# Optimization experiments

Measured on AMD Instinct MI355X. Metric: run time of the kernel, lower is better.

## Reference

```python
import jax, jax.numpy as jnp
import numpy as np

B, S, D = 4, 1024, 1024
H = 16
DH = D // H  # head dim = 64
SCALE = DH ** -0.5
NEG = -1e18


def setup_inputs() -> dict:
    key = jax.random.key(0)
    ks = jax.random.split(key, 8)
    queries = jax.random.normal(ks[0], (B, S, D), dtype=jnp.float32)
    keys_ = jax.random.normal(ks[1], (B, S, D), dtype=jnp.float32)
    values = jax.random.normal(ks[2], (B, S, D), dtype=jnp.float32)
    mask = jax.random.randint(ks[3], (B, 1, S), 0, 2).astype(bool)
    sd = 1.0 / np.sqrt(D)
    Wq = jax.random.normal(ks[4], (D, D), dtype=jnp.float32) * sd
    Wk = jax.random.normal(ks[5], (D, D), dtype=jnp.float32) * sd
    Wv = jax.random.normal(ks[6], (D, D), dtype=jnp.float32) * sd
    Wo = jax.random.normal(ks[7], (D, D), dtype=jnp.float32) * sd
    return {"queries": queries, "keys": keys_, "values": values,
            "Wq": Wq, "Wk": Wk, "Wv": Wv, "Wo": Wo, "mask": mask}


def _split_heads(x):
    # [B,S,D] -> [B,H,S,DH]
    b, s, d = x.shape
    return x.reshape(b, s, H, d // H).transpose(0, 2, 1, 3)


def reference(queries, keys, values, Wq, Wk, Wv, Wo, mask):
    q = _split_heads(queries @ Wq) * SCALE          # [B,H,S,DH]
    k = _split_heads(keys @ Wk)                     # [B,H,S,DH]
    v = _split_heads(values @ Wv)                   # [B,H,S,DH]
    logits = jnp.einsum('bhqd,bhkd->bhqk', q, k)    # [B,H,S,S]
    # mask [B,1,Lk] -> unsqueeze head dim -> broadcast over [B,H,Lq,Lk]
    logits = jnp.where(mask[:, None, :, :], NEG, logits)
    attention_weights = logits.sum(axis=1) / H      # [B,S,S] head-averaged logits
    w = jax.nn.softmax(logits, axis=-1)             # dropout p=0 -> identity
    ctx = jnp.einsum('bhqk,bhkd->bhqd', w, v)       # [B,H,S,DH]
    ctx = ctx.transpose(0, 2, 1, 3).reshape(q.shape[0], q.shape[2], H * DH)
    outputs = ctx @ Wo                              # [B,S,D]
    return (outputs, attention_weights)
```

## Files before the change

kernel.cpp:

```cpp
#include <hip/hip_runtime.h>
#include <hip/hip_bf16.h>

typedef __bf16 bf16;
typedef __attribute__((ext_vector_type(8))) __bf16 bf16x8;
typedef __attribute__((ext_vector_type(4))) __bf16 bf16x4;
typedef __attribute__((ext_vector_type(4))) float f32x4;

#define NEGV (-1e18f)
#define LOG2E 1.4426950408889634f

__device__ __forceinline__ bf16 f2b(float f) {
    unsigned u = __builtin_bit_cast(unsigned, f);
    u += 0x7fffu + ((u >> 16) & 1u);
    unsigned short h = (unsigned short)(u >> 16);
    return __builtin_bit_cast(bf16, h);
}

__device__ __forceinline__ f32x4 mfma16(bf16x8 a, bf16x8 b, f32x4 c) {
    return __builtin_amdgcn_mfma_f32_16x16x32_bf16(a, b, c, 0, 0, 0);
}

__device__ __forceinline__ void gl16(const void* g, void* l) {
    __builtin_amdgcn_global_load_lds((const __attribute__((address_space(1))) void*)g,
                                     (__attribute__((address_space(3))) void*)l, 16, 0, 0);
}

__global__ __launch_bounds__(256) void wconv(const float* __restrict__ W0,
                                             const float* __restrict__ W1,
                                             const float* __restrict__ W2,
                                             const float* __restrict__ W3,
                                             bf16* __restrict__ out) {
    __shared__ float tile[64][65];
    const float* Ws[4] = {W0, W1, W2, W3};
    const float* W = Ws[blockIdx.z];
    bf16* O = out + ((size_t)blockIdx.z << 20);
    int t = threadIdx.x;
    int k0 = blockIdx.x * 64, n0 = blockIdx.y * 64;
#pragma unroll
    for (int p = 0; p < 4; p++) {
        int r = (t >> 4) + p * 16, c = (t & 15) * 4;
        float4 v = *(const float4*)&W[(size_t)(k0 + r) * 1024 + n0 + c];
        tile[r][c] = v.x; tile[r][c + 1] = v.y; tile[r][c + 2] = v.z; tile[r][c + 3] = v.w;
    }
    __syncthreads();
#pragma unroll
    for (int p = 0; p < 4; p++) {
        int r = (t >> 4) + p * 16, c = (t & 15) * 4;
        bf16x4 o;
        o[0] = f2b(tile[c][r]); o[1] = f2b(tile[c + 1][r]);
        o[2] = f2b(tile[c + 2][r]); o[3] = f2b(tile[c + 3][r]);
        *(bf16x4*)&O[(size_t)(n0 + r) * 1024 + k0 + c] = o;
    }
}

__global__ __launch_bounds__(256, 3) void gemm_proj(const float* __restrict__ Qf,
                                                    const float* __restrict__ Kf,
                                                    const float* __restrict__ Vf,
                                                    const bf16* __restrict__ WtQ,
                                                    bf16* __restrict__ Qw,
                                                    bf16* __restrict__ Kw,
                                                    bf16* __restrict__ VtG) {
    __shared__ bf16 As[128 * 64];
    __shared__ bf16 Bs[128 * 64];
    char* AsB = (char*)As;
    char* BsB = (char*)Bs;
    int t = threadIdx.x;
    int m0 = blockIdx.x * 128, n0 = blockIdx.y * 128;
    int z = blockIdx.z;
    const float* A = (z == 0) ? Qf : (z == 1) ? Kf : Vf;
    const bf16* Bt = WtQ + ((size_t)z << 20);
    int wid = t >> 6, lane = t & 63;
    int wr = wid >> 1, wc = wid & 1, lr = lane & 15, lg = lane >> 4;
    f32x4 zero = {0.f, 0.f, 0.f, 0.f};
    f32x4 acc[4][4];
#pragma unroll
    for (int m = 0; m < 4; m++)
#pragma unroll
        for (int n = 0; n < 4; n++) acc[m][n] = zero;

    float4 pa[4][2];
#pragma unroll
    for (int i = 0; i < 4; i++) {
        int c = wid * 256 + i * 64 + lane;
        int row = c >> 3, q = c & 7;
        const float* src = &A[(size_t)(m0 + row) * 1024 + q * 8];
        pa[i][0] = *(const float4*)src;
        pa[i][1] = *(const float4*)(src + 4);
    }

    for (int k0 = 0; k0 < 1024; k0 += 64) {
        __syncthreads();
#pragma unroll
        for (int i = 0; i < 4; i++) {
            int c = wid * 256 + i * 64 + lane;
            int row = c >> 3, q = (c & 7) ^ (row & 7);
            gl16(&Bt[(size_t)(n0 + row) * 1024 + k0 + q * 8], (void*)&Bs[c * 8]);
        }
#pragma unroll
        for (int i = 0; i < 4; i++) {
            int c = wid * 256 + i * 64 + lane;
            int row = c >> 3;
            bf16x8 o;
            o[0] = f2b(pa[i][0].x); o[1] = f2b(pa[i][0].y);
            o[2] = f2b(pa[i][0].z); o[3] = f2b(pa[i][0].w);
            o[4] = f2b(pa[i][1].x); o[5] = f2b(pa[i][1].y);
            o[6] = f2b(pa[i][1].z); o[7] = f2b(pa[i][1].w);
            *(bf16x8*)(AsB + ((c * 16) ^ ((row & 7) << 4))) = o;
        }
        __syncthreads();
        if (k0 < 960) {
#pragma unroll
            for (int i = 0; i < 4; i++) {
                int c = wid * 256 + i * 64 + lane;
                int row = c >> 3, q = c & 7;
                const float* src = &A[(size_t)(m0 + row) * 1024 + k0 + 64 + q * 8];
                pa[i][0] = *(const float4*)src;
                pa[i][1] = *(const float4*)(src + 4);
            }
        }
#pragma unroll
        for (int kk = 0; kk < 2; kk++) {
            bf16x8 af[4], bfr[4];
#pragma unroll
            for (int m = 0; m < 4; m++) {
                int row = wr * 64 + m * 16 + lr;
                af[m] = *(const bf16x8*)(AsB + ((row * 128 + kk * 64 + lg * 16) ^ ((row & 7) << 4)));
            }
#pragma unroll
            for (int n = 0; n < 4; n++) {
                int row = wc * 64 + n * 16 + lr;
                bfr[n] = *(const bf16x8*)(BsB + ((row * 128 + kk * 64 + lg * 16) ^ ((row & 7) << 4)));
            }
#pragma unroll
            for (int m = 0; m < 4; m++)
#pragma unroll
                for (int n = 0; n < 4; n++) acc[m][n] = mfma16(af[m], bfr[n], acc[m][n]);
        }
    }
#pragma unroll
    for (int n = 0; n < 4; n++) {
        int colg = n0 + wc * 64 + n * 16 + lr;
#pragma unroll
        for (int m = 0; m < 4; m++) {
            int rowg = m0 + wr * 64 + m * 16 + lg * 4;
            if (z == 2) {
                bf16x4 o;
#pragma unroll
                for (int j = 0; j < 4; j++) o[j] = f2b(acc[m][n][j]);
                *(bf16x4*)&VtG[(size_t)colg * 4096 + rowg] = o;
            } else {
                bf16* C = (z == 0) ? Qw : Kw;
                float sc = (z == 0) ? 0.125f : 1.0f;
#pragma unroll
                for (int j = 0; j < 4; j++)
                    C[(size_t)(rowg + j) * 1024 + colg] = f2b(acc[m][n][j] * sc);
            }
        }
    }
}

__global__ __launch_bounds__(256, 3) void gemm_oa(const bf16* __restrict__ CTX,
                                                  const bf16* __restrict__ WtO,
                                                  float* __restrict__ out,
                                                  const bf16* __restrict__ Qw,
                                                  const bf16* __restrict__ Kw,
                                                  float* __restrict__ aw,
                                                  const int* __restrict__ maskp) {
    __shared__ bf16 As[128 * 64];
    __shared__ bf16 Bs[128 * 64];
    char* AsB = (char*)As;
    char* BsB = (char*)Bs;
    int t = threadIdx.x;
    int z = blockIdx.z;
    int bx = blockIdx.x;
    int m0, n0 = blockIdx.y * 128;
    const bf16* A;
    const bf16* Bt;
    float* C;
    const int* mask = nullptr;
    if (z == 0) {
        m0 = bx * 128;
        A = CTX; Bt = WtO; C = out;
    } else {
        int b = bx >> 3;
        m0 = (bx & 7) * 128;
        A = Qw + ((size_t)b << 20); Bt = Kw + ((size_t)b << 20);
        C = aw + ((size_t)b << 20); mask = maskp + b * 1024;
    }
    int wid = t >> 6, lane = t & 63;
    int wr = wid >> 1, wc = wid & 1, lr = lane & 15, lg = lane >> 4;
    f32x4 zero = {0.f, 0.f, 0.f, 0.f};
    f32x4 acc[4][4];
#pragma unroll
    for (int m = 0; m < 4; m++)
#pragma unroll
        for (int n = 0; n < 4; n++) acc[m][n] = zero;

    for (int k0 = 0; k0 < 1024; k0 += 64) {
        __syncthreads();
#pragma unroll
        for (int i = 0; i < 4; i++) {
            int c = wid * 256 + i * 64 + lane;
            int row = c >> 3, q = (c & 7) ^ (row & 7);
            gl16(&A[(size_t)(m0 + row) * 1024 + k0 + q * 8], (void*)&As[c * 8]);
            gl16(&Bt[(size_t)(n0 + row) * 1024 + k0 + q * 8], (void*)&Bs[c * 8]);
        }
        __syncthreads();
#pragma unroll
        for (int kk = 0; kk < 2; kk++) {
            bf16x8 af[4], bfr[4];
#pragma unroll
            for (int m = 0; m < 4; m++) {
                int row = wr * 64 + m * 16 + lr;
                af[m] = *(const bf16x8*)(AsB + ((row * 128 + kk * 64 + lg * 16) ^ ((row & 7) << 4)));
            }
#pragma unroll
            for (int n = 0; n < 4; n++) {
                int row = wc * 64 + n * 16 + lr;
                bfr[n] = *(const bf16x8*)(BsB + ((row * 128 + kk * 64 + lg * 16) ^ ((row & 7) << 4)));
            }
#pragma unroll
            for (int m = 0; m < 4; m++)
#pragma unroll
                for (int n = 0; n < 4; n++) acc[m][n] = mfma16(af[m], bfr[n], acc[m][n]);
        }
    }
#pragma unroll
    for (int n = 0; n < 4; n++) {
        int colg = n0 + wc * 64 + n * 16 + lr;
        int mk = (z == 1) ? mask[colg] : 0;
#pragma unroll
        for (int m = 0; m < 4; m++) {
            int rowg = m0 + wr * 64 + m * 16 + lg * 4;
#pragma unroll
            for (int j = 0; j < 4; j++) {
                float v = acc[m][n][j];
                size_t idx = (size_t)(rowg + j) * 1024 + colg;
                if (z == 0) C[idx] = v;
                else C[idx] = mk ? NEGV : v * (1.f / 16.f);
            }
        }
    }
}

__global__ __launch_bounds__(256, 4) void flash_k(const bf16* __restrict__ Q,
                                                  const bf16* __restrict__ K,
                                                  const bf16* __restrict__ VT,
                                                  bf16* __restrict__ CTX,
                                                  const int* __restrict__ maskp) {
    __shared__ bf16 Ks[64 * 64];
    __shared__ bf16 Vs[64 * 64];
    __shared__ bf16 Ps[4][16 * 64];
    __shared__ float biasS[1024];
    int bid = blockIdx.x;
    int qt = bid & 15, h = (bid >> 4) & 15, b = bid >> 8;
    int t = threadIdx.x, wid = t >> 6, lane = t & 63;
    int lr = lane & 15, lg = lane >> 4;
    int qbase = qt * 64 + wid * 16;
    const size_t bS = (size_t)b * 1024;
    char* KsB = (char*)Ks;
    char* VsB = (char*)Vs;
    char* PsW = (char*)&Ps[wid][0];
    const int sxl = (lr & 7) << 4;

    {
        int4 mv = *(const int4*)&maskp[b * 1024 + t * 4];
        float4 bv;
        const float NB = NEGV * LOG2E;
        bv.x = mv.x ? NB : 0.f; bv.y = mv.y ? NB : 0.f;
        bv.z = mv.z ? NB : 0.f; bv.w = mv.w ? NB : 0.f;
        *(float4*)&biasS[t * 4] = bv;
    }

    bf16x8 qf[2];
#pragma unroll
    for (int c = 0; c < 2; c++)
        qf[c] = *(const bf16x8*)&Q[(bS + qbase + lr) * 1024 + h * 64 + c * 32 + lg * 8];

    f32x4 zero = {0.f, 0.f, 0.f, 0.f};
    f32x4 acc[4];
#pragma unroll
    for (int d = 0; d < 4; d++) acc[d] = zero;
    float mr = -INFINITY;
    float lsum = 0.f;

    const bf16* Kbase = K + bS * 1024 + h * 64;
    const bf16* Vbase = VT + (size_t)(h * 64) * 4096 + bS;

    int c0 = t, c1 = t + 256;
    int kr0 = c0 >> 3, kq0 = c0 & 7, kr1 = c1 >> 3, kq1 = c1 & 7;

    bf16x8 kg[2], vg[2];
    kg[0] = *(const bf16x8*)&Kbase[(size_t)kr0 * 1024 + kq0 * 8];
    kg[1] = *(const bf16x8*)&Kbase[(size_t)kr1 * 1024 + kq1 * 8];
    vg[0] = *(const bf16x8*)&Vbase[(size_t)kr0 * 4096 + kq0 * 8];
    vg[1] = *(const bf16x8*)&Vbase[(size_t)kr1 * 4096 + kq1 * 8];

    for (int kt = 0; kt < 16; kt++) {
        __syncthreads();
        *(bf16x8*)(KsB + ((kr0 * 128 + kq0 * 16) ^ ((kr0 & 7) << 4))) = kg[0];
        *(bf16x8*)(KsB + ((kr1 * 128 + kq1 * 16) ^ ((kr1 & 7) << 4))) = kg[1];
        *(bf16x8*)(VsB + ((kr0 * 128 + kq0 * 16) ^ ((kr0 & 7) << 4))) = vg[0];
        *(bf16x8*)(VsB + ((kr1 * 128 + kq1 * 16) ^ ((kr1 & 7) << 4))) = vg[1];
        __syncthreads();
        if (kt < 15) {
            size_t ko = (size_t)(kt + 1) * 64;
            kg[0] = *(const bf16x8*)&Kbase[(ko + kr0) * 1024 + kq0 * 8];
            kg[1] = *(const bf16x8*)&Kbase[(ko + kr1) * 1024 + kq1 * 8];
            vg[0] = *(const bf16x8*)&Vbase[(size_t)kr0 * 4096 + ko + kq0 * 8];
            vg[1] = *(const bf16x8*)&Vbase[(size_t)kr1 * 4096 + ko + kq1 * 8];
        }
        f32x4 s[4];
        __builtin_amdgcn_s_setprio(1);
#pragma unroll
        for (int n = 0; n < 4; n++) {
            int row = n * 16 + lr;
            bf16x8 kf0 = *(const bf16x8*)(KsB + ((row * 128 + lg * 16) ^ sxl));
            bf16x8 kf1 = *(const bf16x8*)(KsB + ((row * 128 + 64 + lg * 16) ^ sxl));
            f32x4 zz = zero;
            zz = mfma16(kf0, qf[0], zz);
            zz = mfma16(kf1, qf[1], zz);
            s[n] = zz;
        }
        __builtin_amdgcn_s_setprio(0);
#pragma unroll
        for (int n = 0; n < 4; n++) {
            float4 bv = *(const float4*)&biasS[kt * 64 + n * 16 + lg * 4];
            s[n][0] = __builtin_fmaf(s[n][0], LOG2E, bv.x);
            s[n][1] = __builtin_fmaf(s[n][1], LOG2E, bv.y);
            s[n][2] = __builtin_fmaf(s[n][2], LOG2E, bv.z);
            s[n][3] = __builtin_fmaf(s[n][3], LOG2E, bv.w);
        }
        float pm;
        {
            float a0 = fmaxf(fmaxf(s[0][0], s[0][1]), fmaxf(s[0][2], s[0][3]));
            float a1 = fmaxf(fmaxf(s[1][0], s[1][1]), fmaxf(s[1][2], s[1][3]));
            float a2 = fmaxf(fmaxf(s[2][0], s[2][1]), fmaxf(s[2][2], s[2][3]));
            float a3 = fmaxf(fmaxf(s[3][0], s[3][1]), fmaxf(s[3][2], s[3][3]));
            pm = fmaxf(fmaxf(a0, a1), fmaxf(a2, a3));
        }
        pm = fmaxf(pm, __shfl_xor(pm, 16));
        pm = fmaxf(pm, __shfl_xor(pm, 32));
        float mn = fmaxf(mr, pm);
        float sc = __builtin_exp2f(mr - mn);
        mr = mn;
        float rs;
        {
            float r0 = 0.f, r1 = 0.f, r2 = 0.f, r3 = 0.f;
#pragma unroll
            for (int n = 0; n < 4; n++) {
                float p0 = __builtin_exp2f(s[n][0] - mn);
                float p1 = __builtin_exp2f(s[n][1] - mn);
                float p2 = __builtin_exp2f(s[n][2] - mn);
                float p3 = __builtin_exp2f(s[n][3] - mn);
                s[n][0] = p0; s[n][1] = p1; s[n][2] = p2; s[n][3] = p3;
                r0 += p0; r1 += p1; r2 += p2; r3 += p3;
            }
            rs = (r0 + r1) + (r2 + r3);
        }
        rs += __shfl_xor(rs, 16);
        rs += __shfl_xor(rs, 32);
        lsum = lsum * sc + rs;
        float scb[4];
#pragma unroll
        for (int j = 0; j < 4; j++) scb[j] = __shfl(sc, lg * 4 + j);
#pragma unroll
        for (int d = 0; d < 4; d++) {
            acc[d][0] *= scb[0]; acc[d][1] *= scb[1];
            acc[d][2] *= scb[2]; acc[d][3] *= scb[3];
        }
#pragma unroll
        for (int n = 0; n < 4; n++) {
            bf16x4 o;
            o[0] = (bf16)s[n][0]; o[1] = (bf16)s[n][1];
            o[2] = (bf16)s[n][2]; o[3] = (bf16)s[n][3];
            *(bf16x4*)(PsW + ((lr * 128 + n * 32 + lg * 8) ^ sxl)) = o;
        }
        __builtin_amdgcn_s_setprio(1);
#pragma unroll
        for (int c = 0; c < 2; c++) {
            bf16x8 pa = *(const bf16x8*)(PsW + ((lr * 128 + c * 64 + lg * 16) ^ sxl));
#pragma unroll
            for (int d = 0; d < 4; d++) {
                int row = d * 16 + lr;
                bf16x8 vb = *(const bf16x8*)(VsB + ((row * 128 + c * 64 + lg * 16) ^ ((row & 7) << 4)));
                acc[d] = mfma16(pa, vb, acc[d]);
            }
        }
        __builtin_amdgcn_s_setprio(0);
    }
    float lb[4];
#pragma unroll
    for (int j = 0; j < 4; j++) lb[j] = __shfl(lsum, lg * 4 + j);
#pragma unroll
    for (int j = 0; j < 4; j++) {
        float inv = 1.f / lb[j];
#pragma unroll
        for (int d = 0; d < 4; d++)
            CTX[(bS + qbase + lg * 4 + j) * 1024 + h * 64 + d * 16 + lr] = f2b(acc[d][j] * inv);
    }
}

extern "C" void kernel_launch(void* const* d_in, const int* in_sizes, int n_in,
                              void* d_out, int out_size, void* d_ws, size_t ws_size,
                              hipStream_t stream) {
    const float* queries = (const float*)d_in[0];
    const float* keys    = (const float*)d_in[1];
    const float* values  = (const float*)d_in[2];
    const float* Wq = (const float*)d_in[3];
    const float* Wk = (const float*)d_in[4];
    const float* Wv = (const float*)d_in[5];
    const float* Wo = (const float*)d_in[6];
    const int* mask = (const int*)d_in[7];

    float* out = (float*)d_out;
    float* aw  = out + ((size_t)4 << 20);

    bf16* wsb = (bf16*)d_ws;
    bf16* WtQ = wsb;
    bf16* Qw  = wsb + ((size_t)4 << 20);
    bf16* Kw  = wsb + ((size_t)8 << 20);
    bf16* VtG = wsb + ((size_t)12 << 20);
    bf16* CTX = wsb + ((size_t)16 << 20);

    wconv<<<dim3(16, 16, 4), 256, 0, stream>>>(Wq, Wk, Wv, Wo, WtQ);
    gemm_proj<<<dim3(32, 8, 3), 256, 0, stream>>>(queries, keys, values, WtQ, Qw, Kw, VtG);
    flash_k<<<dim3(1024), 256, 0, stream>>>(Qw, Kw, VtG, CTX, mask);
    gemm_oa<<<dim3(32, 8, 2), 256, 0, stream>>>(CTX, WtQ + ((size_t)3 << 20), out,
                                                Qw, Kw, aw, mask);
}
```

Baseline: 116.8 us.

## Double-buffer LDS tiles in projection and output GEMMs to overlap loads with MFMA

Both GEMM kernels now keep two LDS buffers for the A and B tiles. The next k-tile is staged into the alternate buffer while MFMAs run on the current one, which leaves one barrier per iteration instead of two. The extra shared memory lowers the launch-bounds occupancy hint from 3 to 2 blocks per CU. Overlap should hide global-to-LDS latency, at the cost of fewer resident waves.

```diff
diff --git a/kernel.cpp b/kernel.cpp
--- a/kernel.cpp
+++ b/kernel.cpp
@@ -53,17 +53,18 @@
     }
 }
 
-__global__ __launch_bounds__(256, 3) void gemm_proj(const float* __restrict__ Qf,
+__global__ __launch_bounds__(256, 2) void gemm_proj(const float* __restrict__ Qf,
                                                     const float* __restrict__ Kf,
                                                     const float* __restrict__ Vf,
                                                     const bf16* __restrict__ WtQ,
                                                     bf16* __restrict__ Qw,
                                                     bf16* __restrict__ Kw,
                                                     bf16* __restrict__ VtG) {
-    __shared__ bf16 As[128 * 64];
-    __shared__ bf16 Bs[128 * 64];
+    __shared__ bf16 As[2][128 * 64];
+    __shared__ bf16 Bs[2][128 * 64];
     char* AsB = (char*)As;
     char* BsB = (char*)Bs;
+    const int BUFSZ = 128 * 64 * 2;
     int t = threadIdx.x;
     int m0 = blockIdx.x * 128, n0 = blockIdx.y * 128;
     int z = blockIdx.z;
@@ -78,45 +79,55 @@
 #pragma unroll
         for (int n = 0; n < 4; n++) acc[m][n] = zero;
 
-    float4 pa[4][2];
+    int sc_[4], srow[4], sq[4];
 #pragma unroll
     for (int i = 0; i < 4; i++) {
         int c = wid * 256 + i * 64 + lane;
-        int row = c >> 3, q = c & 7;
-        const float* src = &A[(size_t)(m0 + row) * 1024 + q * 8];
-        pa[i][0] = *(const float4*)src;
-        pa[i][1] = *(const float4*)(src + 4);
-    }
-
+        sc_[i] = c; srow[i] = c >> 3; sq[i] = c & 7;
+    }
+
+    float4 pa[4][2];
+#define LOADA(K0)                                                              \
+    {                                                                          \
+        _Pragma("unroll") for (int i = 0; i < 4; i++) {                        \
+            const float* src = &A[(size_t)(m0 + srow[i]) * 1024 + (K0) + sq[i] * 8]; \
+            pa[i][0] = *(const float4*)src;                                    \
+            pa[i][1] = *(const float4*)(src + 4);                              \
+        }                                                                      \
+    }
+#define STAGE_B(BUF, K0)                                                       \
+    {                                                                          \
+        _Pragma("unroll") for (int i = 0; i < 4; i++) {                        \
+            int q = sq[i] ^ (srow[i] & 7);                                     \
+            gl16(&Bt[(size_t)(n0 + srow[i]) * 1024 + (K0) + q * 8],            \
+                 (void*)&Bs[BUF][sc_[i] * 8]);                                 \
+        }                                                                      \
+    }
+#define WRITE_A(BUF)                                                           \
+    {                                                                          \
+        _Pragma("unroll") for (int i = 0; i < 4; i++) {                        \
+            bf16x8 o;                                                          \
+            o[0] = f2b(pa[i][0].x); o[1] = f2b(pa[i][0].y);                    \
+            o[2] = f2b(pa[i][0].z); o[3] = f2b(pa[i][0].w);                    \
+            o[4] = f2b(pa[i][1].x); o[5] = f2b(pa[i][1].y);                    \
+            o[6] = f2b(pa[i][1].z); o[7] = f2b(pa[i][1].w);                    \
+            *(bf16x8*)(AsB + (BUF) * BUFSZ +                                   \
+                       ((sc_[i] * 16) ^ ((srow[i] & 7) << 4))) = o;            \
+        }                                                                      \
+    }
+
+    LOADA(0);
+    STAGE_B(0, 0);
+    WRITE_A(0);
+    LOADA(64);
+    __syncthreads();
+
+    int cur = 0;
     for (int k0 = 0; k0 < 1024; k0 += 64) {
-        __syncthreads();
-#pragma unroll
-        for (int i = 0; i < 4; i++) {
-            int c = wid * 256 + i * 64 + lane;
-            int row = c >> 3, q = (c & 7) ^ (row & 7);
-            gl16(&Bt[(size_t)(n0 + row) * 1024 + k0 + q * 8], (void*)&Bs[c * 8]);
-        }
-#pragma unroll
-        for (int i = 0; i < 4; i++) {
-            int c = wid * 256 + i * 64 + lane;
-            int row = c >> 3;
-            bf16x8 o;
-            o[0] = f2b(pa[i][0].x); o[1] = f2b(pa[i][0].y);
-            o[2] = f2b(pa[i][0].z); o[3] = f2b(pa[i][0].w);
-            o[4] = f2b(pa[i][1].x); o[5] = f2b(pa[i][1].y);
-            o[6] = f2b(pa[i][1].z); o[7] = f2b(pa[i][1].w);
-            *(bf16x8*)(AsB + ((c * 16) ^ ((row & 7) << 4))) = o;
-        }
-        __syncthreads();
         if (k0 < 960) {
-#pragma unroll
-            for (int i = 0; i < 4; i++) {
-                int c = wid * 256 + i * 64 + lane;
-                int row = c >> 3, q = c & 7;
-                const float* src = &A[(size_t)(m0 + row) * 1024 + k0 + 64 + q * 8];
-                pa[i][0] = *(const float4*)src;
-                pa[i][1] = *(const float4*)(src + 4);
-            }
+            STAGE_B(cur ^ 1, k0 + 64);
+            WRITE_A(cur ^ 1);
+            if (k0 < 896) LOADA(k0 + 128);
         }
 #pragma unroll
         for (int kk = 0; kk < 2; kk++) {
@@ -124,19 +135,26 @@
 #pragma unroll
             for (int m = 0; m < 4; m++) {
                 int row = wr * 64 + m * 16 + lr;
-                af[m] = *(const bf16x8*)(AsB + ((row * 128 + kk * 64 + lg * 16) ^ ((row & 7) << 4)));
+                af[m] = *(const bf16x8*)(AsB + cur * BUFSZ +
+                                         ((row * 128 + kk * 64 + lg * 16) ^ ((row & 7) << 4)));
             }
 #pragma unroll
             for (int n = 0; n < 4; n++) {
                 int row = wc * 64 + n * 16 + lr;
-                bfr[n] = *(const bf16x8*)(BsB + ((row * 128 + kk * 64 + lg * 16) ^ ((row & 7) << 4)));
+                bfr[n] = *(const bf16x8*)(BsB + cur * BUFSZ +
+                                          ((row * 128 + kk * 64 + lg * 16) ^ ((row & 7) << 4)));
             }
 #pragma unroll
             for (int m = 0; m < 4; m++)
 #pragma unroll
                 for (int n = 0; n < 4; n++) acc[m][n] = mfma16(af[m], bfr[n], acc[m][n]);
         }
-    }
+        __syncthreads();
+        cur ^= 1;
+    }
+#undef LOADA
+#undef STAGE_B
+#undef WRITE_A
 #pragma unroll
     for (int n = 0; n < 4; n++) {
         int colg = n0 + wc * 64 + n * 16 + lr;
@@ -159,17 +177,18 @@
     }
 }
 
-__global__ __launch_bounds__(256, 3) void gemm_oa(const bf16* __restrict__ CTX,
+__global__ __launch_bounds__(256, 2) void gemm_oa(const bf16* __restrict__ CTX,
                                                   const bf16* __restrict__ WtO,
                                                   float* __restrict__ out,
                                                   const bf16* __restrict__ Qw,
                                                   const bf16* __restrict__ Kw,
                                                   float* __restrict__ aw,
                                                   const int* __restrict__ maskp) {
-    __shared__ bf16 As[128 * 64];
-    __shared__ bf16 Bs[128 * 64];
+    __shared__ bf16 As[2][128 * 64];
+    __shared__ bf16 Bs[2][128 * 64];
     char* AsB = (char*)As;
     char* BsB = (char*)Bs;
+    const int BUFSZ = 128 * 64 * 2;
     int t = threadIdx.x;
     int z = blockIdx.z;
     int bx = blockIdx.x;
@@ -196,35 +215,51 @@
 #pragma unroll
         for (int n = 0; n < 4; n++) acc[m][n] = zero;
 
+    int sc_[4], srow[4], sqx[4];
+#pragma unroll
+    for (int i = 0; i < 4; i++) {
+        int c = wid * 256 + i * 64 + lane;
+        sc_[i] = c; srow[i] = c >> 3; sqx[i] = (c & 7) ^ ((c >> 3) & 7);
+    }
+#define STAGE_AB(BUF, K0)                                                      \
+    {                                                                          \
+        _Pragma("unroll") for (int i = 0; i < 4; i++) {                        \
+            gl16(&A[(size_t)(m0 + srow[i]) * 1024 + (K0) + sqx[i] * 8],        \
+                 (void*)&As[BUF][sc_[i] * 8]);                                 \
+            gl16(&Bt[(size_t)(n0 + srow[i]) * 1024 + (K0) + sqx[i] * 8],       \
+                 (void*)&Bs[BUF][sc_[i] * 8]);                                 \
+        }                                                                      \
+    }
+
+    STAGE_AB(0, 0);
+    __syncthreads();
+    int cur = 0;
     for (int k0 = 0; k0 < 1024; k0 += 64) {
-        __syncthreads();
-#pragma unroll
-        for (int i = 0; i < 4; i++) {
-            int c = wid * 256 + i * 64 + lane;
-            int row = c >> 3, q = (c & 7) ^ (row & 7);
-            gl16(&A[(size_t)(m0 + row) * 1024 + k0 + q * 8], (void*)&As[c * 8]);
-            gl16(&Bt[(size_t)(n0 + row) * 1024 + k0 + q * 8], (void*)&Bs[c * 8]);
-        }
-        __syncthreads();
+        if (k0 < 960) STAGE_AB(cur ^ 1, k0 + 64);
 #pragma unroll
         for (int kk = 0; kk < 2; kk++) {
             bf16x8 af[4], bfr[4];
 #pragma unroll
             for (int m = 0; m < 4; m++) {
                 int row = wr * 64 + m * 16 + lr;
-                af[m] = *(const bf16x8*)(AsB + ((row * 128 + kk * 64 + lg * 16) ^ ((row & 7) << 4)));
+                af[m] = *(const bf16x8*)(AsB + cur * BUFSZ +
+                                         ((row * 128 + kk * 64 + lg * 16) ^ ((row & 7) << 4)));
             }
 #pragma unroll
             for (int n = 0; n < 4; n++) {
                 int row = wc * 64 + n * 16 + lr;
-                bfr[n] = *(const bf16x8*)(BsB + ((row * 128 + kk * 64 + lg * 16) ^ ((row & 7) << 4)));
+                bfr[n] = *(const bf16x8*)(BsB + cur * BUFSZ +
+                                          ((row * 128 + kk * 64 + lg * 16) ^ ((row & 7) << 4)));
             }
 #pragma unroll
             for (int m = 0; m < 4; m++)
 #pragma unroll
                 for (int n = 0; n < 4; n++) acc[m][n] = mfma16(af[m], bfr[n], acc[m][n]);
         }
-    }
+        __syncthreads();
+        cur ^= 1;
+    }
+#undef STAGE_AB
 #pragma unroll
     for (int n = 0; n < 4; n++) {
         int colg = n0 + wc * 64 + n * 16 + lr;
```

Result: slower. 124.0 us (+6.2%).

## Pre-convert QKV inputs to bf16 and use 256x256 ping-pong pipelined projection GEMM

Applied to the files above, without the earlier changes.

Adds a separate conversion kernel that turns the fp32 query/key/value activations into bf16 buffers, reusing the attention-weights output region and a workspace slot as scratch. The projection GEMM becomes a 512-thread kernel with 256x256 tiles, double-buffered LDS filled via direct global-to-LDS loads, and explicit barrier/setprio phases that interleave staging with MFMA work. The aim is higher data reuse and better overlap of loads with compute. In exchange it adds an extra launch and a full fp32-read/bf16-write pass, and the grid shrinks to 192 blocks at one block per CU, which may leave some CUs idle.

```diff
diff --git a/kernel.cpp b/kernel.cpp
--- a/kernel.cpp
+++ b/kernel.cpp
@@ -53,96 +53,163 @@
     }
 }
 
-__global__ __launch_bounds__(256, 3) void gemm_proj(const float* __restrict__ Qf,
-                                                    const float* __restrict__ Kf,
-                                                    const float* __restrict__ Vf,
-                                                    const bf16* __restrict__ WtQ,
-                                                    bf16* __restrict__ Qw,
-                                                    bf16* __restrict__ Kw,
-                                                    bf16* __restrict__ VtG) {
-    __shared__ bf16 As[128 * 64];
-    __shared__ bf16 Bs[128 * 64];
-    char* AsB = (char*)As;
-    char* BsB = (char*)Bs;
+__global__ __launch_bounds__(256) void cvt3(const float* __restrict__ Qf,
+                                            const float* __restrict__ Kf,
+                                            const float* __restrict__ Vf,
+                                            bf16* __restrict__ Qa,
+                                            bf16* __restrict__ Ka,
+                                            bf16* __restrict__ Va) {
+    int z = blockIdx.y;
+    const float* in = (z == 0) ? Qf : (z == 1) ? Kf : Vf;
+    bf16* out = (z == 0) ? Qa : (z == 1) ? Ka : Va;
+    size_t i = ((size_t)blockIdx.x * 256 + threadIdx.x) * 8;
+    float4 a = *(const float4*)&in[i];
+    float4 b = *(const float4*)&in[i + 4];
+    bf16x8 o;
+    o[0] = f2b(a.x); o[1] = f2b(a.y); o[2] = f2b(a.z); o[3] = f2b(a.w);
+    o[4] = f2b(b.x); o[5] = f2b(b.y); o[6] = f2b(b.z); o[7] = f2b(b.w);
+    *(bf16x8*)&out[i] = o;
+}
+
+__global__ __launch_bounds__(512, 1) void gemm8(const bf16* __restrict__ Qa,
+                                                const bf16* __restrict__ Ka,
+                                                const bf16* __restrict__ Va,
+                                                const bf16* __restrict__ WtQ,
+                                                bf16* __restrict__ Qw,
+                                                bf16* __restrict__ Kw,
+                                                bf16* __restrict__ VtG) {
+    __shared__ bf16 LA[2][256 * 64];
+    __shared__ bf16 LB[2][256 * 64];
+    char* LAB = (char*)LA;
+    char* LBB = (char*)LB;
     int t = threadIdx.x;
-    int m0 = blockIdx.x * 128, n0 = blockIdx.y * 128;
     int z = blockIdx.z;
-    const float* A = (z == 0) ? Qf : (z == 1) ? Kf : Vf;
+    const bf16* A = (z == 0) ? Qa : (z == 1) ? Ka : Va;
     const bf16* Bt = WtQ + ((size_t)z << 20);
+    int m0 = blockIdx.x * 256, n0 = blockIdx.y * 256;
     int wid = t >> 6, lane = t & 63;
-    int wr = wid >> 1, wc = wid & 1, lr = lane & 15, lg = lane >> 4;
+    int wr = wid >> 2, wc = wid & 3, lr = lane & 15, lg = lane >> 4;
+    const int sxl = (lr & 7) << 4;
+    const int arow = wr * 128 + lr;
+    const int brow = wc * 64 + lr;
+    const int c0 = t, c1 = t + 512;
+    const int r0 = c0 >> 3, q0 = (c0 & 7) ^ (r0 & 7);
+    const int r1 = c1 >> 3, q1 = (c1 & 7) ^ (r1 & 7);
+
     f32x4 zero = {0.f, 0.f, 0.f, 0.f};
-    f32x4 acc[4][4];
-#pragma unroll
-    for (int m = 0; m < 4; m++)
+    f32x4 acc[8][4];
+#pragma unroll
+    for (int m = 0; m < 8; m++)
 #pragma unroll
         for (int n = 0; n < 4; n++) acc[m][n] = zero;
-
-    float4 pa[4][2];
-#pragma unroll
-    for (int i = 0; i < 4; i++) {
-        int c = wid * 256 + i * 64 + lane;
-        int row = c >> 3, q = c & 7;
-        const float* src = &A[(size_t)(m0 + row) * 1024 + q * 8];
-        pa[i][0] = *(const float4*)src;
-        pa[i][1] = *(const float4*)(src + 4);
-    }
-
-    for (int k0 = 0; k0 < 1024; k0 += 64) {
-        __syncthreads();
-#pragma unroll
-        for (int i = 0; i < 4; i++) {
-            int c = wid * 256 + i * 64 + lane;
-            int row = c >> 3, q = (c & 7) ^ (row & 7);
-            gl16(&Bt[(size_t)(n0 + row) * 1024 + k0 + q * 8], (void*)&Bs[c * 8]);
-        }
-#pragma unroll
-        for (int i = 0; i < 4; i++) {
-            int c = wid * 256 + i * 64 + lane;
-            int row = c >> 3;
-            bf16x8 o;
-            o[0] = f2b(pa[i][0].x); o[1] = f2b(pa[i][0].y);
-            o[2] = f2b(pa[i][0].z); o[3] = f2b(pa[i][0].w);
-            o[4] = f2b(pa[i][1].x); o[5] = f2b(pa[i][1].y);
-            o[6] = f2b(pa[i][1].z); o[7] = f2b(pa[i][1].w);
-            *(bf16x8*)(AsB + ((c * 16) ^ ((row & 7) << 4))) = o;
-        }
-        __syncthreads();
-        if (k0 < 960) {
-#pragma unroll
-            for (int i = 0; i < 4; i++) {
-                int c = wid * 256 + i * 64 + lane;
-                int row = c >> 3, q = c & 7;
-                const float* src = &A[(size_t)(m0 + row) * 1024 + k0 + 64 + q * 8];
-                pa[i][0] = *(const float4*)src;
-                pa[i][1] = *(const float4*)(src + 4);
-            }
-        }
-#pragma unroll
-        for (int kk = 0; kk < 2; kk++) {
-            bf16x8 af[4], bfr[4];
-#pragma unroll
-            for (int m = 0; m < 4; m++) {
-                int row = wr * 64 + m * 16 + lr;
-                af[m] = *(const bf16x8*)(AsB + ((row * 128 + kk * 64 + lg * 16) ^ ((row & 7) << 4)));
-            }
-#pragma unroll
-            for (int n = 0; n < 4; n++) {
-                int row = wc * 64 + n * 16 + lr;
-                bfr[n] = *(const bf16x8*)(BsB + ((row * 128 + kk * 64 + lg * 16) ^ ((row & 7) << 4)));
-            }
-#pragma unroll
-            for (int m = 0; m < 4; m++)
-#pragma unroll
-                for (int n = 0; n < 4; n++) acc[m][n] = mfma16(af[m], bfr[n], acc[m][n]);
-        }
-    }
-#pragma unroll
-    for (int n = 0; n < 4; n++) {
-        int colg = n0 + wc * 64 + n * 16 + lr;
-#pragma unroll
-        for (int m = 0; m < 4; m++) {
-            int rowg = m0 + wr * 64 + m * 16 + lg * 4;
+    bf16x8 a[4][2], b0[2][2], b1[2][2];
+
+#define STG_A(BUF, HALF, KT)                                                   \
+    gl16(&A[(size_t)(m0 + (HALF) * 128 + r0) * 1024 + (KT) * 64 + q0 * 8],     \
+         (void*)(LAB + (BUF) * 32768 + (HALF) * 16384 + c0 * 16));             \
+    gl16(&A[(size_t)(m0 + (HALF) * 128 + r1) * 1024 + (KT) * 64 + q1 * 8],     \
+         (void*)(LAB + (BUF) * 32768 + (HALF) * 16384 + c1 * 16));
+#define STG_B(BUF, HALF, KT)                                                   \
+    gl16(&Bt[(size_t)(n0 + (HALF) * 128 + r0) * 1024 + (KT) * 64 + q0 * 8],    \
+         (void*)(LBB + (BUF) * 32768 + (HALF) * 16384 + c0 * 16));             \
+    gl16(&Bt[(size_t)(n0 + (HALF) * 128 + r1) * 1024 + (KT) * 64 + q1 * 8],    \
+         (void*)(LBB + (BUF) * 32768 + (HALF) * 16384 + c1 * 16));
+#define RD_A(BUF, MH)                                                          \
+    {                                                                          \
+        _Pragma("unroll") for (int m = 0; m < 4; m++) {                        \
+            int row = arow + (MH) * 64 + m * 16;                               \
+            _Pragma("unroll") for (int ks = 0; ks < 2; ks++)                   \
+                a[m][ks] = *(const bf16x8*)(LAB + (BUF) * 32768 +              \
+                           ((row * 128 + ks * 64 + lg * 16) ^ sxl));           \
+        }                                                                      \
+    }
+#define RD_B(BUF, NH, DST)                                                     \
+    {                                                                          \
+        _Pragma("unroll") for (int n = 0; n < 2; n++) {                        \
+            int row = brow + (NH) * 32 + n * 16;                               \
+            _Pragma("unroll") for (int ks = 0; ks < 2; ks++)                   \
+                DST[n][ks] = *(const bf16x8*)(LBB + (BUF) * 32768 +            \
+                             ((row * 128 + ks * 64 + lg * 16) ^ sxl));         \
+        }                                                                      \
+    }
+#define MM(MH, NH, BB)                                                         \
+    {                                                                          \
+        _Pragma("unroll") for (int m = 0; m < 4; m++)                          \
+        _Pragma("unroll") for (int n = 0; n < 2; n++)                          \
+        _Pragma("unroll") for (int ks = 0; ks < 2; ks++)                       \
+            acc[(MH) * 4 + m][(NH) * 2 + n] =                                  \
+                mfma16(a[m][ks], BB[n][ks], acc[(MH) * 4 + m][(NH) * 2 + n]);  \
+    }
+#define PH_PRE                                                                 \
+    __builtin_amdgcn_s_barrier();                                              \
+    asm volatile("s_waitcnt lgkmcnt(0)" ::: "memory");                         \
+    __builtin_amdgcn_sched_barrier(0);                                         \
+    __builtin_amdgcn_s_setprio(1);
+#define PH_POST                                                                \
+    __builtin_amdgcn_s_setprio(0);                                             \
+    __builtin_amdgcn_s_barrier();
+
+    STG_A(0, 0, 0); STG_A(0, 1, 0); STG_B(0, 0, 0); STG_B(0, 1, 0);
+    STG_A(1, 0, 1); STG_B(1, 0, 1); STG_B(1, 1, 1);
+    asm volatile("s_waitcnt vmcnt(6)" ::: "memory");
+    __builtin_amdgcn_s_barrier();
+
+    for (int i = 0; i < 7; i++) {
+        int kt = 2 * i;
+        RD_A(0, 0); RD_B(0, 0, b0); STG_A(1, 1, kt + 1);
+        PH_PRE; MM(0, 0, b0); PH_POST;
+        RD_B(0, 1, b1); STG_A(0, 0, kt + 2);
+        PH_PRE; MM(0, 1, b1); PH_POST;
+        RD_A(0, 1); STG_B(0, 0, kt + 2);
+        PH_PRE; MM(1, 0, b0); PH_POST;
+        STG_B(0, 1, kt + 2);
+        PH_PRE; MM(1, 1, b1);
+        __builtin_amdgcn_s_setprio(0);
+        asm volatile("s_waitcnt vmcnt(6)" ::: "memory");
+        __builtin_amdgcn_s_barrier();
+        RD_A(1, 0); RD_B(1, 0, b0); STG_A(0, 1, kt + 2);
+        PH_PRE; MM(0, 0, b0); PH_POST;
+        RD_B(1, 1, b1); STG_A(1, 0, kt + 3);
+        PH_PRE; MM(0, 1, b1); PH_POST;
+        RD_A(1, 1); STG_B(1, 0, kt + 3);
+        PH_PRE; MM(1, 0, b0); PH_POST;
+        STG_B(1, 1, kt + 3);
+        PH_PRE; MM(1, 1, b1);
+        __builtin_amdgcn_s_setprio(0);
+        asm volatile("s_waitcnt vmcnt(6)" ::: "memory");
+        __builtin_amdgcn_s_barrier();
+    }
+    RD_A(0, 0); RD_B(0, 0, b0); STG_A(1, 1, 15);
+    PH_PRE; MM(0, 0, b0); PH_POST;
+    RD_B(0, 1, b1);
+    PH_PRE; MM(0, 1, b1); PH_POST;
+    RD_A(0, 1);
+    PH_PRE; MM(1, 0, b0); PH_POST;
+    PH_PRE; MM(1, 1, b1);
+    __builtin_amdgcn_s_setprio(0);
+    asm volatile("s_waitcnt vmcnt(0)" ::: "memory");
+    __builtin_amdgcn_s_barrier();
+    RD_A(1, 0); RD_B(1, 0, b0);
+    PH_PRE; MM(0, 0, b0); PH_POST;
+    RD_B(1, 1, b1);
+    PH_PRE; MM(0, 1, b1); PH_POST;
+    RD_A(1, 1);
+    PH_PRE; MM(1, 0, b0); PH_POST;
+    PH_PRE; MM(1, 1, b1);
+    __builtin_amdgcn_s_setprio(0);
+#undef STG_A
+#undef STG_B
+#undef RD_A
+#undef RD_B
+#undef MM
+#undef PH_PRE
+#undef PH_POST
+#pragma unroll
+    for (int m = 0; m < 8; m++) {
+        int rowg = m0 + wr * 128 + m * 16 + lg * 4;
+#pragma unroll
+        for (int n = 0; n < 4; n++) {
+            int colg = n0 + wc * 64 + n * 16 + lr;
             if (z == 2) {
                 bf16x4 o;
 #pragma unroll
@@ -418,13 +485,17 @@
 
     bf16* wsb = (bf16*)d_ws;
     bf16* WtQ = wsb;
-    bf16* Qw  = wsb + ((size_t)4 << 20);
-    bf16* Kw  = wsb + ((size_t)8 << 20);
-    bf16* VtG = wsb + ((size_t)12 << 20);
-    bf16* CTX = wsb + ((size_t)16 << 20);
+    bf16* Qa  = wsb + ((size_t)4 << 20);
+    bf16* Qw  = wsb + ((size_t)8 << 20);
+    bf16* Kw  = wsb + ((size_t)12 << 20);
+    bf16* VtG = wsb + ((size_t)16 << 20);
+    bf16* Ka  = (bf16*)aw;
+    bf16* Va  = (bf16*)aw + ((size_t)4 << 20);
+    bf16* CTX = Qa;
 
     wconv<<<dim3(16, 16, 4), 256, 0, stream>>>(Wq, Wk, Wv, Wo, WtQ);
-    gemm_proj<<<dim3(32, 8, 3), 256, 0, stream>>>(queries, keys, values, WtQ, Qw, Kw, VtG);
+    cvt3<<<dim3(2048, 3), 256, 0, stream>>>(queries, keys, values, Qa, Ka, Va);
+    gemm8<<<dim3(16, 4, 3), 512, 0, stream>>>(Qa, Ka, Va, WtQ, Qw, Kw, VtG);
     flash_k<<<dim3(1024), 256, 0, stream>>>(Qw, Kw, VtG, CTX, mask);
     gemm_oa<<<dim3(32, 8, 2), 256, 0, stream>>>(CTX, WtQ + ((size_t)3 << 20), out,
                                                 Qw, Kw, aw, mask);
```

Result: slower. 125.5 us (+7.4%).
